# Optimization experiments

Hardware: AMD Instinct MI355X
Metric: run time of the kernel (lower is better)

## Reference

```python
import jax, jax.numpy as jnp
import numpy as np

DIM = 1024
B, S = 4, 2048

def setup_inputs() -> dict:
    key = jax.random.key(0)
    ks = jax.random.split(key, 4)
    x = jax.random.normal(ks[0], (B, S, DIM), dtype=jnp.float32)
    mask = jax.random.randint(ks[1], (B, S, S), 0, 2, dtype=jnp.int32)
    Wqkv = jax.random.normal(ks[2], (DIM, 3 * DIM), dtype=jnp.float32) / np.sqrt(DIM)
    bqkv = jnp.zeros((3 * DIM,), dtype=jnp.float32)
    Wout = jax.random.normal(ks[3], (DIM, DIM), dtype=jnp.float32) / np.sqrt(DIM)
    bout = jnp.zeros((DIM,), dtype=jnp.float32)
    return {"x": x, "mask": mask, "Wqkv": Wqkv, "bqkv": bqkv, "Wout": Wout, "bout": bout}

def reference(x, mask, Wqkv, bqkv, Wout, bout):
    dim = x.shape[-1]
    qkv = x @ Wqkv + bqkv                      # [B,S,3*dim]
    q, k, v = jnp.split(qkv, 3, axis=-1)       # each [B,S,dim]
    scores = jnp.einsum('bqd,bkd->bqk', q, k) / jnp.sqrt(jnp.float32(dim))
    # faithful to torch: masked positions set to 1e-10 (NOT -inf)
    scores = jnp.where(mask == 0, jnp.float32(1e-10), scores)
    attn = jax.nn.softmax(scores, axis=-1)     # dropout is identity in eval
    out = jnp.einsum('bqk,bkd->bqd', attn, v)  # [B,S,dim]
    return out @ Wout + bout
```

## Files before the change

### kernel.cpp

```cpp
#include <hip/hip_runtime.h>


typedef __attribute__((ext_vector_type(8))) short short8;
typedef __attribute__((ext_vector_type(4))) float f32x4;
typedef unsigned short u16;

#define SEQ 2048
#define NB 4

static __device__ __forceinline__ u16 f2bf(float f) {
    unsigned int u = __builtin_bit_cast(unsigned int, f);
    u += 0x7fffu + ((u >> 16) & 1u);
    return (u16)(u >> 16);
}
static __device__ __forceinline__ float bf2f(u16 h) {
    unsigned int u = ((unsigned int)h) << 16;
    return __builtin_bit_cast(float, u);
}

static __device__ __forceinline__ void gld16(const u16* l, const u16* g) {
    __builtin_amdgcn_global_load_lds(
        (__attribute__((address_space(1))) void*)(g),
        (__attribute__((address_space(3))) void*)(l),
        16, 0, 0);
}

__global__ __launch_bounds__(256) void cvt_bf16(const float* __restrict__ s,
                                                u16* __restrict__ d, long n) {
    long i = ((long)blockIdx.x * 256 + threadIdx.x) * 8;
    if (i >= n) return;
    f32x4 a = *(const f32x4*)(s + i);
    f32x4 b = *(const f32x4*)(s + i + 4);
    short8 o;
    o[0] = (short)f2bf(a.x); o[1] = (short)f2bf(a.y);
    o[2] = (short)f2bf(a.z); o[3] = (short)f2bf(a.w);
    o[4] = (short)f2bf(b.x); o[5] = (short)f2bf(b.y);
    o[6] = (short)f2bf(b.z); o[7] = (short)f2bf(b.w);
    *(short8*)(d + i) = o;
}

__global__ __launch_bounds__(256) void transpose_cvt(const float* __restrict__ in,
                                                     u16* __restrict__ out,
                                                     int R, int C) {
    __shared__ float t[32][33];
    const int c0 = blockIdx.x * 32;
    const int r0 = blockIdx.y * 32;
    const int x = threadIdx.x & 31;
    const int y = (threadIdx.x >> 5) * 4;
    #pragma unroll
    for (int i = 0; i < 4; i++)
        t[y + i][x] = in[(long)(r0 + y + i) * C + c0 + x];
    __syncthreads();
    #pragma unroll
    for (int i = 0; i < 4; i++)
        out[(long)(c0 + y + i) * R + r0 + x] = f2bf(t[x][y + i]);
}

__global__ __launch_bounds__(256) void transpose_v(const u16* __restrict__ qkv,
                                                   u16* __restrict__ vt) {
    __shared__ u16 t[32][33];
    const int b = blockIdx.z;
    const int s0 = blockIdx.y * 32;
    const int d0 = blockIdx.x * 32;
    const int x = threadIdx.x & 31;
    const int y = (threadIdx.x >> 5) * 4;
    const u16* src = qkv + (long)b * SEQ * 3072 + 2048;
    u16* dst = vt + (long)b * 1024 * SEQ;
    #pragma unroll
    for (int i = 0; i < 4; i++)
        t[y + i][x] = src[(long)(s0 + y + i) * 3072 + d0 + x];
    __syncthreads();
    #pragma unroll
    for (int i = 0; i < 4; i++)
        dst[(long)(d0 + y + i) * SEQ + s0 + x] = t[x][y + i];
}

template<int EPI>
__global__ __launch_bounds__(512) void gemm256(
    const u16* __restrict__ Ap, long lda, long aBatch,
    const u16* __restrict__ Bp, long ldb, long bBatch,
    void* __restrict__ Cp, long ldc, long cBatch,
    const float* __restrict__ bias, float scale, int K, int nbx)
{
    __shared__ __attribute__((aligned(16))) u16 lds[2][4][8192];

    const int T = K >> 6;
    const int tid = threadIdx.x;
    const int lane = tid & 63;
    const int wave = tid >> 6;
    const int wm = wave >> 2;
    const int wn = wave & 3;
    const int m16 = lane & 15;
    const int quad = lane >> 4;
    const int b = blockIdx.z;

    const int nwg = gridDim.x;
    int wg = blockIdx.x;
    if ((nwg & 7) == 0)
        wg = (wg & 7) * (nwg >> 3) + (wg >> 3);
    const int bx = wg % nbx;
    const int by = wg / nbx;
    const long gm0 = (long)by * 256;
    const long gn0 = (long)bx * 256;

    const u16* A = Ap + (long)b * aBatch;
    const u16* B = Bp + (long)b * bBatch;

    const int rl = lane >> 3;
    const int lsl = ((lane & 7) ^ rl) * 8;
    const long aR = gm0 + wave * 8 + rl;
    const long bR = gn0 + (wave >> 2) * 64 + (wave & 3) * 8 + rl;

#define STG_A(bufi, h, tt) do { \
    const long kc_ = (long)((((tt) < T) ? (tt) : (tt) - 2) << 6); \
    gld16(&lds[bufi][h][wave * 512],       A + (aR + (h) * 64) * lda + kc_ + lsl); \
    gld16(&lds[bufi][h][(8 + wave) * 512], A + (aR + 128 + (h) * 64) * lda + kc_ + lsl); \
} while (0)
#define STG_B(bufi, h, tt) do { \
    const long kc_ = (long)((((tt) < T) ? (tt) : (tt) - 2) << 6); \
    gld16(&lds[bufi][2 + (h)][wave * 512],       B + (bR + (h) * 32) * ldb + kc_ + lsl); \
    gld16(&lds[bufi][2 + (h)][(8 + wave) * 512], B + (bR + 128 + (h) * 32) * ldb + kc_ + lsl); \
} while (0)

    const int s0 = quad ^ (m16 & 7);
    const int aBase = (wm * 64 + m16) * 64;
    const int bBase = (wn * 32 + m16) * 64;
    const int aoff0 = aBase + s0 * 8, aoff1 = aBase + (s0 ^ 4) * 8;
    const int boff0 = bBase + s0 * 8, boff1 = bBase + (s0 ^ 4) * 8;

    short8 aF[4][2], b0F[2][2], b1F[2][2];
    f32x4 acc[8][4];
    #pragma unroll
    for (int mi = 0; mi < 8; mi++)
        #pragma unroll
        for (int ni = 0; ni < 4; ni++)
            acc[mi][ni] = (f32x4){0.f, 0.f, 0.f, 0.f};

#define LD_A(bufi, h) do { \
    const u16* p_ = &lds[bufi][h][0]; \
    _Pragma("unroll") \
    for (int mfl_ = 0; mfl_ < 4; ++mfl_) { \
        aF[mfl_][0] = *(const short8*)(p_ + aoff0 + mfl_ * 1024); \
        aF[mfl_][1] = *(const short8*)(p_ + aoff1 + mfl_ * 1024); \
    } \
} while (0)
#define LD_B(bufi, h, BF) do { \
    const u16* p_ = &lds[bufi][2 + (h)][0]; \
    _Pragma("unroll") \
    for (int nj_ = 0; nj_ < 2; ++nj_) { \
        BF[nj_][0] = *(const short8*)(p_ + boff0 + nj_ * 1024); \
        BF[nj_][1] = *(const short8*)(p_ + boff1 + nj_ * 1024); \
    } \
} while (0)
#define MFMAQ(mh, nh, BF) do { \
    _Pragma("unroll") \
    for (int mi_ = 0; mi_ < 4; ++mi_) \
    _Pragma("unroll") \
    for (int nj_ = 0; nj_ < 2; ++nj_) { \
        acc[(mh)*4+mi_][(nh)*2+nj_] = __builtin_amdgcn_mfma_f32_16x16x32_bf16( \
            aF[mi_][0], BF[nj_][0], acc[(mh)*4+mi_][(nh)*2+nj_], 0, 0, 0); \
        acc[(mh)*4+mi_][(nh)*2+nj_] = __builtin_amdgcn_mfma_f32_16x16x32_bf16( \
            aF[mi_][1], BF[nj_][1], acc[(mh)*4+mi_][(nh)*2+nj_], 0, 0, 0); \
    } \
} while (0)
#define BAR() __builtin_amdgcn_s_barrier()
#define LGKM0() asm volatile("s_waitcnt lgkmcnt(0)" ::: "memory")
#define VM6() asm volatile("s_waitcnt vmcnt(6)" ::: "memory")

    STG_A(0, 0, 0);
    STG_B(0, 0, 0);
    STG_B(0, 1, 0);
    STG_A(0, 1, 0);
    STG_A(1, 0, 1);
    STG_B(1, 0, 1);
    VM6();
    BAR();

    for (int t = 0; t < T; ++t) {
        const int buf = t & 1, nb = buf ^ 1;
        LD_A(buf, 0);
        LD_B(buf, 0, b0F);
        STG_B(nb, 1, t + 1);
        BAR(); LGKM0();
        __builtin_amdgcn_s_setprio(1);
        MFMAQ(0, 0, b0F);
        __builtin_amdgcn_s_setprio(0);
        BAR();
        LD_B(buf, 1, b1F);
        STG_A(nb, 1, t + 1);
        VM6();
        BAR(); LGKM0();
        __builtin_amdgcn_s_setprio(1);
        MFMAQ(0, 1, b1F);
        __builtin_amdgcn_s_setprio(0);
        BAR();
        LD_A(buf, 1);
        STG_A(buf, 0, t + 2);
        BAR(); LGKM0();
        __builtin_amdgcn_s_setprio(1);
        MFMAQ(1, 0, b0F);
        __builtin_amdgcn_s_setprio(0);
        BAR();
        STG_B(buf, 0, t + 2);
        VM6();
        BAR(); LGKM0();
        __builtin_amdgcn_s_setprio(1);
        MFMAQ(1, 1, b1F);
        __builtin_amdgcn_s_setprio(0);
        BAR();
    }

    const long row0 = gm0 + wm * 128 + quad * 4;
    if (EPI == 0 || EPI == 1) {
        u16* C = (u16*)Cp + (long)b * cBatch;
        #pragma unroll
        for (int ni = 0; ni < 4; ++ni) {
            const long col = gn0 + wn * 64 + (ni >> 1) * 32 + (ni & 1) * 16 + m16;
            const float bv = (EPI == 0 && bias) ? bias[col] : 0.f;
            #pragma unroll
            for (int mi = 0; mi < 8; ++mi) {
                const long rb = row0 + (mi >> 2) * 64 + (mi & 3) * 16;
                #pragma unroll
                for (int r = 0; r < 4; ++r) {
                    const float vv = (EPI == 1) ? acc[mi][ni][r] * scale
                                                : acc[mi][ni][r] + bv;
                    C[(rb + r) * ldc + col] = f2bf(vv);
                }
            }
        }
    } else {
        float* C = (float*)Cp + (long)b * cBatch;
        #pragma unroll
        for (int ni = 0; ni < 4; ++ni) {
            const long col = gn0 + wn * 64 + (ni >> 1) * 32 + (ni & 1) * 16 + m16;
            const float bv = bias ? bias[col] : 0.f;
            #pragma unroll
            for (int mi = 0; mi < 8; ++mi) {
                const long rb = row0 + (mi >> 2) * 64 + (mi & 3) * 16;
                #pragma unroll
                for (int r = 0; r < 4; ++r)
                    C[(rb + r) * ldc + col] = acc[mi][ni][r] + bv;
            }
        }
    }
#undef STG_A
#undef STG_B
#undef LD_A
#undef LD_B
#undef MFMAQ
#undef BAR
#undef LGKM0
#undef VM6
}

template<int EPI>
__global__ __launch_bounds__(256) void gemm128(
    const u16* __restrict__ Ap, long lda, long aBatch,
    const u16* __restrict__ Bp, long ldb, long bBatch,
    void* __restrict__ Cp, long ldc, long cBatch,
    const float* __restrict__ bias,
    float scale, int K)
{
    __shared__ __attribute__((aligned(16))) u16 As[128 * 64];
    __shared__ __attribute__((aligned(16))) u16 Bs[128 * 64];

    const int tid = threadIdx.x;
    const int lane = tid & 63;
    const int wave = tid >> 6;
    const int b = blockIdx.z;
    const long m0 = (long)blockIdx.y * 128;
    const long n0 = (long)blockIdx.x * 128;

    const u16* A = Ap + (long)b * aBatch;
    const u16* B = Bp + (long)b * bBatch;

    const int wm = (wave >> 1) * 64;
    const int wn = (wave & 1) * 64;
    const int m16 = lane & 15;
    const int quad = lane >> 4;

    const int srow = lane >> 3;
    const int skk = (lane & 7) * 8;

    f32x4 acc[4][4];
    #pragma unroll
    for (int mi = 0; mi < 4; mi++)
        #pragma unroll
        for (int ni = 0; ni < 4; ni++)
            acc[mi][ni] = (f32x4){0.f, 0.f, 0.f, 0.f};

    for (int k0 = 0; k0 < K; k0 += 64) {
        #pragma unroll
        for (int c = 0; c < 4; c++) {
            const int r = wave * 32 + c * 8 + srow;
            gld16(As + (wave * 4 + c) * 512, A + (m0 + r) * lda + k0 + skk);
            gld16(Bs + (wave * 4 + c) * 512, B + (n0 + r) * ldb + k0 + skk);
        }
        __syncthreads();

        #pragma unroll
        for (int ks = 0; ks < 2; ks++) {
            short8 af[4], bf[4];
            #pragma unroll
            for (int i = 0; i < 4; i++) {
                af[i] = *(const short8*)&As[(wm + i * 16 + m16) * 64 + ks * 32 + quad * 8];
                bf[i] = *(const short8*)&Bs[(wn + i * 16 + m16) * 64 + ks * 32 + quad * 8];
            }
            #pragma unroll
            for (int mi = 0; mi < 4; mi++)
                #pragma unroll
                for (int ni = 0; ni < 4; ni++)
                    acc[mi][ni] = __builtin_amdgcn_mfma_f32_16x16x32_bf16(
                        af[mi], bf[ni], acc[mi][ni], 0, 0, 0);
        }
        __syncthreads();
    }

    const long row_base = m0 + wm + quad * 4;
    if (EPI == 0) {
        u16* C = (u16*)Cp + (long)b * cBatch;
        #pragma unroll
        for (int ni = 0; ni < 4; ni++) {
            const long col = n0 + wn + ni * 16 + m16;
            const float bv = bias ? bias[col] : 0.f;
            #pragma unroll
            for (int mi = 0; mi < 4; mi++)
                #pragma unroll
                for (int r = 0; r < 4; r++)
                    C[(row_base + mi * 16 + r) * ldc + col] = f2bf(acc[mi][ni][r] + bv);
        }
    } else if (EPI == 1) {
        u16* C = (u16*)Cp + (long)b * cBatch;
        #pragma unroll
        for (int ni = 0; ni < 4; ni++) {
            const long col = n0 + wn + ni * 16 + m16;
            #pragma unroll
            for (int mi = 0; mi < 4; mi++)
                #pragma unroll
                for (int r = 0; r < 4; r++)
                    C[(row_base + mi * 16 + r) * ldc + col] = f2bf(acc[mi][ni][r] * scale);
        }
    } else {
        float* C = (float*)Cp + (long)b * cBatch;
        #pragma unroll
        for (int ni = 0; ni < 4; ni++) {
            const long col = n0 + wn + ni * 16 + m16;
            const float bv = bias ? bias[col] : 0.f;
            #pragma unroll
            for (int mi = 0; mi < 4; mi++)
                #pragma unroll
                for (int r = 0; r < 4; r++)
                    C[(row_base + mi * 16 + r) * ldc + col] = acc[mi][ni][r] + bv;
        }
    }
}

__global__ __launch_bounds__(256) void softmax2048(u16* __restrict__ S,
                                                   const int* __restrict__ mask) {
    const long row = blockIdx.x;
    u16* p = S + row * SEQ;
    const int* mrow = mask + row * SEQ;
    const int tid = threadIdx.x;

    short8 v = *(const short8*)(p + tid * 8);
    uint4 mw0 = *(const uint4*)(mrow + tid * 8);
    uint4 mw1 = *(const uint4*)(mrow + tid * 8 + 4);
    const unsigned int* mwv = (const unsigned int*)&mw0;

    float f[8];
    #pragma unroll
    for (int j = 0; j < 8; j++) {
        const unsigned int mv = (j < 4) ? mwv[j] : ((const unsigned int*)&mw1)[j - 4];
        f[j] = (mv == 0u) ? 1e-10f : bf2f((u16)v[j]);
    }

    float m = f[0];
    #pragma unroll
    for (int j = 1; j < 8; j++) m = fmaxf(m, f[j]);
    #pragma unroll
    for (int i = 1; i < 64; i <<= 1) m = fmaxf(m, __shfl_xor(m, i));

    __shared__ float redm[4], reds[4];
    if ((tid & 63) == 0) redm[tid >> 6] = m;
    __syncthreads();
    m = fmaxf(fmaxf(redm[0], redm[1]), fmaxf(redm[2], redm[3]));

    float e[8], s = 0.f;
    #pragma unroll
    for (int j = 0; j < 8; j++) { e[j] = __expf(f[j] - m); s += e[j]; }
    #pragma unroll
    for (int i = 1; i < 64; i <<= 1) s += __shfl_xor(s, i);
    if ((tid & 63) == 0) reds[tid >> 6] = s;
    __syncthreads();
    s = reds[0] + reds[1] + reds[2] + reds[3];

    const float inv = 1.f / s;
    short8 o;
    #pragma unroll
    for (int j = 0; j < 8; j++) o[j] = (short)f2bf(e[j] * inv);
    *(short8*)(p + tid * 8) = o;
}

extern "C" void kernel_launch(void* const* d_in, const int* in_sizes, int n_in,
                              void* d_out, int out_size, void* d_ws, size_t ws_size,
                              hipStream_t stream) {
    const float* x    = (const float*)d_in[0];
    const int*   mask = (const int*)d_in[1];
    const float* Wqkv = (const float*)d_in[2];
    const float* bqkv = (const float*)d_in[3];
    const float* Wout = (const float*)d_in[4];
    const float* bout = (const float*)d_in[5];
    float* out = (float*)d_out;

    char* ws = (char*)d_ws;
    u16* xh   = (u16*)(ws + 0);
    u16* wqt  = (u16*)(ws + 16777216);
    u16* sc   = (u16*)(ws + 0);
    u16* wot  = (u16*)(ws + 33554432);
    u16* qkv  = (u16*)(ws + 35651584);
    u16* attn = (u16*)(ws + 35651584);
    u16* vt   = (u16*)(ws + 85983232);

    cvt_bf16<<<4096, 256, 0, stream>>>(x, xh, 8388608);
    transpose_cvt<<<dim3(96, 32), 256, 0, stream>>>(Wqkv, wqt, 1024, 3072);
    transpose_cvt<<<dim3(32, 32), 256, 0, stream>>>(Wout, wot, 1024, 1024);

    gemm256<0><<<dim3(384, 1, 1), 512, 0, stream>>>(
        xh, 1024, 0, wqt, 1024, 0, qkv, 3072, 0, bqkv, 1.f, 1024, 12);

    transpose_v<<<dim3(32, 64, NB), 256, 0, stream>>>(qkv, vt);

    gemm256<1><<<dim3(64, 1, NB), 512, 0, stream>>>(
        qkv, 3072, (long)SEQ * 3072, qkv + 1024, 3072, (long)SEQ * 3072,
        sc, SEQ, (long)SEQ * SEQ, nullptr, 0.03125f, 1024, 8);

    softmax2048<<<dim3(NB * SEQ), 256, 0, stream>>>(sc, mask);

    gemm128<0><<<dim3(8, 16, NB), 256, 0, stream>>>(
        sc, SEQ, (long)SEQ * SEQ, vt, SEQ, (long)1024 * SEQ,
        attn, 1024, (long)SEQ * 1024, nullptr, 1.f, 2048);

    gemm128<2><<<dim3(8, 64, 1), 256, 0, stream>>>(
        attn, 1024, 0, wot, 1024, 0, out, 1024, 0, bout, 1.f, 1024);
}
```

Measured before the change: 236.7 us.

## Restructure 256x256 GEMM main loop to prefetch two k-tiles ahead

The 256-tile GEMM main loop is reworked. Global-to-LDS staging now targets the slot given by the k-tile parity and issues loads for tile t+2 instead of t+1. The next B fragment is loaded from LDS before the final MFMA quarter, and the explicit lgkmcnt(0) waits are removed in favour of compiler-tracked dependencies. The aim is deeper latency hiding with fewer barriers stalling MFMA issue. The risk is LDS read/write races from the overwrite timing and the changed vmcnt(8) accounting.

```diff
diff --git a/kernel.cpp b/kernel.cpp
--- a/kernel.cpp
+++ b/kernel.cpp
@@ -111,15 +111,19 @@
     const long aR = gm0 + wave * 8 + rl;
     const long bR = gn0 + (wave >> 2) * 64 + (wave & 3) * 8 + rl;
 
-#define STG_A(bufi, h, tt) do { \
-    const long kc_ = (long)((((tt) < T) ? (tt) : (tt) - 2) << 6); \
-    gld16(&lds[bufi][h][wave * 512],       A + (aR + (h) * 64) * lda + kc_ + lsl); \
-    gld16(&lds[bufi][h][(8 + wave) * 512], A + (aR + 128 + (h) * 64) * lda + kc_ + lsl); \
+#define STG_A(h, tt) do { \
+    const int tc_ = ((tt) < T) ? (tt) : (tt) - 2; \
+    const long kc_ = (long)(tc_ << 6); \
+    const int sl_ = tc_ & 1; \
+    gld16(&lds[sl_][h][wave * 512],       A + (aR + (h) * 64) * lda + kc_ + lsl); \
+    gld16(&lds[sl_][h][(8 + wave) * 512], A + (aR + 128 + (h) * 64) * lda + kc_ + lsl); \
 } while (0)
-#define STG_B(bufi, h, tt) do { \
-    const long kc_ = (long)((((tt) < T) ? (tt) : (tt) - 2) << 6); \
-    gld16(&lds[bufi][2 + (h)][wave * 512],       B + (bR + (h) * 32) * ldb + kc_ + lsl); \
-    gld16(&lds[bufi][2 + (h)][(8 + wave) * 512], B + (bR + 128 + (h) * 32) * ldb + kc_ + lsl); \
+#define STG_B(h, tt) do { \
+    const int tc_ = ((tt) < T) ? (tt) : (tt) - 2; \
+    const long kc_ = (long)(tc_ << 6); \
+    const int sl_ = tc_ & 1; \
+    gld16(&lds[sl_][2 + (h)][wave * 512],       B + (bR + (h) * 32) * ldb + kc_ + lsl); \
+    gld16(&lds[sl_][2 + (h)][(8 + wave) * 512], B + (bR + 128 + (h) * 32) * ldb + kc_ + lsl); \
 } while (0)
 
     const int s0 = quad ^ (m16 & 7);
@@ -136,16 +140,16 @@
         for (int ni = 0; ni < 4; ni++)
             acc[mi][ni] = (f32x4){0.f, 0.f, 0.f, 0.f};
 
-#define LD_A(bufi, h) do { \
-    const u16* p_ = &lds[bufi][h][0]; \
+#define LD_A(sl, h) do { \
+    const u16* p_ = &lds[sl][h][0]; \
     _Pragma("unroll") \
     for (int mfl_ = 0; mfl_ < 4; ++mfl_) { \
         aF[mfl_][0] = *(const short8*)(p_ + aoff0 + mfl_ * 1024); \
         aF[mfl_][1] = *(const short8*)(p_ + aoff1 + mfl_ * 1024); \
     } \
 } while (0)
-#define LD_B(bufi, h, BF) do { \
-    const u16* p_ = &lds[bufi][2 + (h)][0]; \
+#define LD_B(sl, h, BF) do { \
+    const u16* p_ = &lds[sl][2 + (h)][0]; \
     _Pragma("unroll") \
     for (int nj_ = 0; nj_ < 2; ++nj_) { \
         BF[nj_][0] = *(const short8*)(p_ + boff0 + nj_ * 1024); \
@@ -163,51 +167,35 @@
             aF[mi_][1], BF[nj_][1], acc[(mh)*4+mi_][(nh)*2+nj_], 0, 0, 0); \
     } \
 } while (0)
-#define BAR() __builtin_amdgcn_s_barrier()
-#define LGKM0() asm volatile("s_waitcnt lgkmcnt(0)" ::: "memory")
-#define VM6() asm volatile("s_waitcnt vmcnt(6)" ::: "memory")
-
-    STG_A(0, 0, 0);
-    STG_B(0, 0, 0);
-    STG_B(0, 1, 0);
-    STG_A(0, 1, 0);
-    STG_A(1, 0, 1);
-    STG_B(1, 0, 1);
-    VM6();
+#define BAR() asm volatile("s_barrier" ::: "memory")
+#define VM8() asm volatile("s_waitcnt vmcnt(8)" ::: "memory")
+#define SETP(p) __builtin_amdgcn_s_setprio(p)
+
+    STG_A(0, 0); STG_B(0, 0); STG_B(1, 0); STG_A(1, 0);
+    STG_A(0, 1); STG_B(0, 1); STG_B(1, 1); STG_A(1, 1);
+    VM8();
     BAR();
+    LD_B(0, 0, b0F);
 
     for (int t = 0; t < T; ++t) {
         const int buf = t & 1, nb = buf ^ 1;
         LD_A(buf, 0);
-        LD_B(buf, 0, b0F);
-        STG_B(nb, 1, t + 1);
-        BAR(); LGKM0();
-        __builtin_amdgcn_s_setprio(1);
-        MFMAQ(0, 0, b0F);
-        __builtin_amdgcn_s_setprio(0);
+        SETP(1); MFMAQ(0, 0, b0F); SETP(0);
         BAR();
         LD_B(buf, 1, b1F);
-        STG_A(nb, 1, t + 1);
-        VM6();
-        BAR(); LGKM0();
-        __builtin_amdgcn_s_setprio(1);
-        MFMAQ(0, 1, b1F);
-        __builtin_amdgcn_s_setprio(0);
+        STG_A(0, t + 2);
+        STG_B(0, t + 2);
+        SETP(1); MFMAQ(0, 1, b1F); SETP(0);
         BAR();
         LD_A(buf, 1);
-        STG_A(buf, 0, t + 2);
-        BAR(); LGKM0();
-        __builtin_amdgcn_s_setprio(1);
-        MFMAQ(1, 0, b0F);
-        __builtin_amdgcn_s_setprio(0);
+        STG_B(1, t + 2);
+        SETP(1); MFMAQ(1, 0, b0F); SETP(0);
         BAR();
-        STG_B(buf, 0, t + 2);
-        VM6();
-        BAR(); LGKM0();
-        __builtin_amdgcn_s_setprio(1);
-        MFMAQ(1, 1, b1F);
-        __builtin_amdgcn_s_setprio(0);
+        STG_A(1, t + 2);
+        VM8();
         BAR();
+        LD_B(nb, 0, b0F);
+        SETP(1); MFMAQ(1, 1, b1F); SETP(0);
     }
 
     const long row0 = gm0 + wm * 128 + quad * 4;
@@ -249,8 +237,8 @@
 #undef LD_B
 #undef MFMAQ
 #undef BAR
-#undef LGKM0
-#undef VM6
+#undef VM8
+#undef SETP
 }
 
 template<int EPI>
```

Result: no change. 236.0 us (-0.3%).
